# Optimization experiments

Measured on AMD Instinct MI355X. Metric: run time of the kernel, lower is better.

The kernel has to match this reference:

```python
import jax, jax.numpy as jnp
import numpy as np

EPS = 1e-5


def _layernorm(x, w, b):
    mu = jnp.mean(x, axis=-1, keepdims=True)
    xc = x - mu
    var = jnp.mean(xc * xc, axis=-1, keepdims=True)
    return xc * jax.lax.rsqrt(var + EPS) * w + b


def _s5_ssm(u, lam_re, lam_im, log_step, B_re, B_im, C_re, C_im, Dvec):
    # u: [B,L,D]; diagonal complex SSM with ZOH discretization + associative scan
    Lam = lam_re + 1j * lam_im                      # [P]
    step = jnp.exp(log_step)                        # [P]
    Abar = jnp.exp(Lam * step)                      # [P]
    Bbar = ((Abar - 1.0) / Lam)[:, None] * (B_re + 1j * B_im)  # [P,D]
    Bu = jnp.einsum('bld,pd->blp', u.astype(jnp.complex64), Bbar)  # [B,L,P]
    A_el = jnp.broadcast_to(Abar, Bu.shape)

    def binop(e1, e2):
        a1, b1 = e1
        a2, b2 = e2
        return a1 * a2, a2 * b1 + b2

    _, xs = jax.lax.associative_scan(binop, (A_el, Bu), axis=1)  # [B,L,P] complex
    y = jnp.einsum('blp,dp->bld', xs, C_re + 1j * C_im).real + Dvec * u
    return y


def _s5_block(x, an_w, an_b, lam_re, lam_im, log_step, B_re, B_im, C_re, C_im,
              Dvec, fn_w, fn_b, Wenc, Wdec):
    fx = _layernorm(x, an_w, an_b)
    s = _s5_ssm(fx, lam_re, lam_im, log_step, B_re, B_im, C_re, C_im, Dvec)
    z = jax.nn.gelu(s, approximate=False) + fx
    fy = _layernorm(z, fn_w, fn_b)
    h = fy @ Wenc.T                                  # [B,L,2D]
    a, g = jnp.split(h, 2, axis=-1)                  # GEGLU
    return (a * jax.nn.gelu(g, approximate=False)) @ Wdec.T + fy


def setup_inputs() -> dict:
    D = 1048   # d_model
    P = 1048   # state_dim
    NL = 3
    Bsz, L = 4, 4096
    key = jax.random.key(0)
    ks = jax.random.split(key, 20)
    f32 = jnp.float32
    inp = {}
    inp['x'] = jax.random.normal(ks[0], (Bsz, L, 1), f32)
    inp['enc_w'] = jax.random.normal(ks[1], (D, 1), f32)
    inp['enc_b'] = jnp.zeros((D,), f32)
    inp['norm_w'] = jnp.ones((NL, D), f32)
    inp['norm_b'] = jnp.zeros((NL, D), f32)
    inp['attn_norm_w'] = jnp.ones((NL, D), f32)
    inp['attn_norm_b'] = jnp.zeros((NL, D), f32)
    inp['ff_norm_w'] = jnp.ones((NL, D), f32)
    inp['ff_norm_b'] = jnp.zeros((NL, D), f32)
    # stable diagonal dynamics: Re(Lambda) < 0
    inp['lam_re'] = -0.5 * jax.random.uniform(ks[2], (NL, P), f32) - 0.05
    inp['lam_im'] = np.float32(np.pi) * jax.random.normal(ks[3], (NL, P), f32)
    lo, hi = np.float32(np.log(1e-3)), np.float32(np.log(1e-1))
    inp['log_step'] = lo + (hi - lo) * jax.random.uniform(ks[4], (NL, P), f32)
    sB = np.float32(1.0 / np.sqrt(D))
    sC = np.float32(1.0 / np.sqrt(P))
    inp['B_re'] = sB * jax.random.normal(ks[5], (NL, P, D), f32)
    inp['B_im'] = sB * jax.random.normal(ks[6], (NL, P, D), f32)
    inp['C_re'] = sC * jax.random.normal(ks[7], (NL, D, P), f32)
    inp['C_im'] = sC * jax.random.normal(ks[8], (NL, D, P), f32)
    inp['Dvec'] = jax.random.normal(ks[9], (NL, D), f32)
    sW = np.float32(1.0 / np.sqrt(D))
    inp['Wenc'] = sW * jax.random.normal(ks[10], (NL, 2 * D, D), f32)
    inp['Wdec'] = sW * jax.random.normal(ks[11], (NL, D, D), f32)
    inp['head_w'] = sW * jax.random.normal(ks[12], (1, D), f32)
    inp['head_b'] = jnp.zeros((1,), f32)
    return inp


def reference(x, enc_w, enc_b, norm_w, norm_b, attn_norm_w, attn_norm_b,
              ff_norm_w, ff_norm_b, lam_re, lam_im, log_step, B_re, B_im,
              C_re, C_im, Dvec, Wenc, Wdec, head_w, head_b):
    h = x @ enc_w.T + enc_b                          # [B,L,D]
    n_layers = norm_w.shape[0]
    for i in range(n_layers):                        # small fixed loop over layers
        z = _layernorm(h, norm_w[i], norm_b[i])      # prenorm
        z = _s5_block(z, attn_norm_w[i], attn_norm_b[i], lam_re[i], lam_im[i],
                      log_step[i], B_re[i], B_im[i], C_re[i], C_im[i],
                      Dvec[i], ff_norm_w[i], ff_norm_b[i], Wenc[i], Wdec[i])
        h = h + z                                    # residual (dropout = identity in eval)
    pooled = jnp.mean(h, axis=1)                     # [B,D]
    y = (pooled @ head_w.T + head_b).squeeze(-1)     # [B]
    return y
```

## Files before the change

### kernel.cpp

```cpp
#include <hip/hip_runtime.h>
#include <hip/hip_bf16.h>
#include <cstddef>

typedef __hip_bfloat16 bf16;

#define D_MODEL 1048
#define P_DIM   1048
#define NLAYER  3
#define BSZ     4
#define LSEQ    4096
#define BL      (BSZ*LSEQ)
#define BLD     ((size_t)BL*D_MODEL)
#define KP      1056
#define NP      1152
#define BLA     ((size_t)BL*KP)
#define NPKP    ((size_t)NP*KP)

#define NC      64
#define CL      (LSEQ/NC)
#define NSCAN   (BSZ*NC*P_DIM)
#define P2      (P_DIM/2)
#define NSCAN2  (BSZ*NC*P2)

typedef __attribute__((ext_vector_type(8))) short short8;
typedef __attribute__((ext_vector_type(4))) float f32x4;

#define TM 128
#define TN 128
#define TK 32
#define TILE_SH (TM*TK)
#define NGEMM   ((BL/TM)*(NP/TN))
#define KSTEPS  (KP/TK)

__device__ __forceinline__ float gelu_f(float x) {
    return 0.5f * x * (1.f + erff(x * 0.70710678118654752f));
}

__device__ __forceinline__ void tile_coords(int id, int& m0, int& n0) {
    int xcd  = id & 7;
    int slot = id >> 3;
    int xg   = slot / 9;
    int j    = slot - xg*9;
    m0 = (xg*8 + xcd) * TM;
    n0 = j * TN;
}

__device__ __forceinline__ void stage_tile(
    const bf16* __restrict__ src, int row0, int k0, short* lds, int tid)
{
#pragma unroll
    for (int c = 0; c < 2; ++c) {
        int chunk = tid + 256*c;
        int r = chunk >> 2;
        int col = ((chunk ^ (r >> 1)) & 3) * 8;
        __builtin_amdgcn_global_load_lds(
            (const __attribute__((address_space(1))) void*)(src + (size_t)(row0 + r)*KP + k0 + col),
            (__attribute__((address_space(3))) void*)(lds + chunk*8), 16, 0, 0);
    }
}

__device__ __forceinline__ void stage512(
    const bf16* __restrict__ src, int row0, int k0, short* lds, int tid)
{
    int r = tid >> 2;
    int col = ((tid ^ (r >> 1)) & 3) * 8;
    __builtin_amdgcn_global_load_lds(
        (const __attribute__((address_space(1))) void*)(src + (size_t)(row0 + r)*KP + k0 + col),
        (__attribute__((address_space(3))) void*)(lds + tid*8), 16, 0, 0);
}

__device__ __forceinline__ void mfma_step1(
    const short* As, const short* Ws, f32x4 (&acc)[4][4],
    int wm, int wn, int row_in, int qs)
{
    short8 a[4], b[4];
#pragma unroll
    for (int i = 0; i < 4; ++i) {
        a[i] = *(const short8*)&As[(wm + i*16 + row_in)*TK + qs];
        b[i] = *(const short8*)&Ws[(wn + i*16 + row_in)*TK + qs];
    }
#pragma unroll
    for (int i = 0; i < 4; ++i)
#pragma unroll
        for (int j = 0; j < 4; ++j)
            acc[i][j] = __builtin_amdgcn_mfma_f32_16x16x32_bf16(a[i], b[j], acc[i][j], 0, 0, 0);
}

template <int MODE>
__global__ __launch_bounds__(512, 4) void gemm2o_k(
    const bf16* __restrict__ A, const bf16* __restrict__ W0,
    const bf16* __restrict__ W1,
    bf16* __restrict__ O0, bf16* __restrict__ O1, int N)
{
    __shared__ __align__(16) short smem[6*TILE_SH];
    short* As  = smem;
    short* W0s = smem + 2*TILE_SH;
    short* W1s = smem + 4*TILE_SH;
    const int tid  = threadIdx.x;
    int m0, n0;
    tile_coords(blockIdx.x, m0, n0);
    const int wave = tid >> 6, lane = tid & 63;
    const int wr = wave >> 2, wc = wave & 3;
    const int wm = wr * 64;
    const int wn = (wc & 1) * 64;
    const bool useW1 = (wc >= 2);
    const int row_in = lane & 15;
    const int qs = (((lane >> 4) ^ (lane >> 1)) & 3) * 8;

    f32x4 acc[4][4] = {};

    stage512(A,  m0, 0,  As,             tid);
    stage512(W0, n0, 0,  W0s,            tid);
    stage512(W1, n0, 0,  W1s,            tid);
    stage512(A,  m0, 32, As  + TILE_SH,  tid);
    stage512(W0, n0, 32, W0s + TILE_SH,  tid);
    stage512(W1, n0, 32, W1s + TILE_SH,  tid);

    for (int s = 0; s < KSTEPS - 1; ++s) {
        asm volatile("s_waitcnt vmcnt(3)" ::: "memory");
        __builtin_amdgcn_s_barrier();
        const int off = (s & 1) * TILE_SH;
        const short* Ws = (useW1 ? W1s : W0s) + off;
        mfma_step1(As + off, Ws, acc, wm, wn, row_in, qs);
        __builtin_amdgcn_s_barrier();
        if (s < KSTEPS - 2) {
            const int k0 = (s + 2) * TK;
            stage512(A,  m0, k0, As  + off, tid);
            stage512(W0, n0, k0, W0s + off, tid);
            stage512(W1, n0, k0, W1s + off, tid);
        }
    }
    asm volatile("s_waitcnt vmcnt(0)" ::: "memory");
    __builtin_amdgcn_s_barrier();
    {
        const int off = ((KSTEPS-1) & 1) * TILE_SH;
        const short* Ws = (useW1 ? W1s : W0s) + off;
        mfma_step1(As + off, Ws, acc, wm, wn, row_in, qs);
    }

    const int quad = lane >> 4;
    if (MODE == 0) {
        bf16* O = useW1 ? O1 : O0;
#pragma unroll
        for (int i = 0; i < 4; ++i) {
#pragma unroll
            for (int j = 0; j < 4; ++j) {
                int n = n0 + wn + j*16 + row_in;
#pragma unroll
                for (int r = 0; r < 4; ++r) {
                    int m = m0 + wm + i*16 + quad*4 + r;
                    size_t o = (size_t)m*KP + n;
                    if (n < N)        O[o] = __float2bfloat16(acc[i][j][r]);
                    else if (n < KP)  O[o] = __float2bfloat16(0.f);
                }
            }
        }
    } else {
        f32x4* xb = (f32x4*)smem;
        const int pp = wr*2 + (wc & 1);
#pragma unroll
        for (int ih = 0; ih < 2; ++ih) {
            __syncthreads();
            if (useW1) {
#pragma unroll
                for (int il = 0; il < 2; ++il)
#pragma unroll
                    for (int j = 0; j < 4; ++j)
                        xb[(((pp*2 + il)*4 + j) << 6) + lane] = acc[2*ih + il][j];
            }
            __syncthreads();
            if (!useW1) {
#pragma unroll
                for (int il = 0; il < 2; ++il) {
                    int i = 2*ih + il;
#pragma unroll
                    for (int j = 0; j < 4; ++j) {
                        f32x4 g = xb[(((pp*2 + il)*4 + j) << 6) + lane];
                        int n = n0 + wn + j*16 + row_in;
#pragma unroll
                        for (int r = 0; r < 4; ++r) {
                            int m = m0 + wm + i*16 + quad*4 + r;
                            size_t o = (size_t)m*KP + n;
                            if (n < N)        O0[o] = __float2bfloat16(acc[i][j][r] * gelu_f(g[r]));
                            else if (n < KP)  O0[o] = __float2bfloat16(0.f);
                        }
                    }
                }
            }
        }
    }
}

__global__ __launch_bounds__(256, 3) void gemmC_k(
    const bf16* __restrict__ A0, const bf16* __restrict__ W0,
    const bf16* __restrict__ A1, const bf16* __restrict__ W1,
    const bf16* __restrict__ fx, const float* __restrict__ dv,
    bf16* __restrict__ O, int N)
{
    __shared__ __align__(16) short As[2][TILE_SH];
    __shared__ __align__(16) short Ws[2][TILE_SH];
    const int tid  = threadIdx.x;
    int m0, n0;
    tile_coords(blockIdx.x, m0, n0);
    const int wave = tid >> 6, lane = tid & 63;
    const int wm = (wave >> 1) * 64, wn = (wave & 1) * 64;
    const int row_in = lane & 15;
    const int qs = (((lane >> 4) ^ (lane >> 1)) & 3) * 8;

    f32x4 acc[4][4] = {};

    const int NST = 2*KSTEPS;
    stage_tile(A0, m0, 0,  As[0], tid);
    stage_tile(W0, n0, 0,  Ws[0], tid);
    stage_tile(A0, m0, 32, As[1], tid);
    stage_tile(W0, n0, 32, Ws[1], tid);

    for (int s = 0; s < NST - 1; ++s) {
        asm volatile("s_waitcnt vmcnt(4)" ::: "memory");
        __builtin_amdgcn_s_barrier();
        mfma_step1(As[s & 1], Ws[s & 1], acc, wm, wn, row_in, qs);
        __builtin_amdgcn_s_barrier();
        if (s < NST - 2) {
            int t = s + 2;
            const bf16* A = (t >= KSTEPS) ? A1 : A0;
            const bf16* W = (t >= KSTEPS) ? W1 : W0;
            int kk = (t >= KSTEPS) ? t - KSTEPS : t;
            stage_tile(A, m0, kk*TK, As[s & 1], tid);
            stage_tile(W, n0, kk*TK, Ws[s & 1], tid);
        }
    }
    asm volatile("s_waitcnt vmcnt(0)" ::: "memory");
    __builtin_amdgcn_s_barrier();
    mfma_step1(As[(NST-1) & 1], Ws[(NST-1) & 1], acc, wm, wn, row_in, qs);

    const int quad = lane >> 4;
#pragma unroll
    for (int i = 0; i < 4; ++i) {
#pragma unroll
        for (int j = 0; j < 4; ++j) {
            int n = n0 + wn + j*16 + row_in;
#pragma unroll
            for (int r = 0; r < 4; ++r) {
                int m = m0 + wm + i*16 + quad*4 + r;
                size_t o = (size_t)m*KP + n;
                if (n < N) {
                    float f = __bfloat162float(fx[o]);
                    float t = acc[i][j][r] + dv[n]*f;
                    O[o] = __float2bfloat16(gelu_f(t) + f);
                } else if (n < KP) {
                    O[o] = __float2bfloat16(0.f);
                }
            }
        }
    }
}

__global__ __launch_bounds__(256, 3) void gemmD_k(
    const bf16* __restrict__ A, const bf16* __restrict__ W,
    const bf16* __restrict__ fy, float* __restrict__ h, int N)
{
    __shared__ __align__(16) short As[2][TILE_SH];
    __shared__ __align__(16) short Ws[2][TILE_SH];
    const int tid  = threadIdx.x;
    int m0, n0;
    tile_coords(blockIdx.x, m0, n0);
    const int wave = tid >> 6, lane = tid & 63;
    const int wm = (wave >> 1) * 64, wn = (wave & 1) * 64;
    const int row_in = lane & 15;
    const int qs = (((lane >> 4) ^ (lane >> 1)) & 3) * 8;

    f32x4 acc[4][4] = {};

    stage_tile(A, m0, 0,  As[0], tid);
    stage_tile(W, n0, 0,  Ws[0], tid);
    stage_tile(A, m0, 32, As[1], tid);
    stage_tile(W, n0, 32, Ws[1], tid);

    for (int s = 0; s < KSTEPS - 1; ++s) {
        asm volatile("s_waitcnt vmcnt(4)" ::: "memory");
        __builtin_amdgcn_s_barrier();
        mfma_step1(As[s & 1], Ws[s & 1], acc, wm, wn, row_in, qs);
        __builtin_amdgcn_s_barrier();
        if (s < KSTEPS - 2) {
            const int k0 = (s + 2) * TK;
            stage_tile(A, m0, k0, As[s & 1], tid);
            stage_tile(W, n0, k0, Ws[s & 1], tid);
        }
    }
    asm volatile("s_waitcnt vmcnt(0)" ::: "memory");
    __builtin_amdgcn_s_barrier();
    mfma_step1(As[(KSTEPS-1) & 1], Ws[(KSTEPS-1) & 1], acc, wm, wn, row_in, qs);

    const int quad = lane >> 4;
#pragma unroll
    for (int i = 0; i < 4; ++i) {
#pragma unroll
        for (int j = 0; j < 4; ++j) {
            int n = n0 + wn + j*16 + row_in;
            if (n >= N) continue;
#pragma unroll
            for (int r = 0; r < 4; ++r) {
                int m = m0 + wm + i*16 + quad*4 + r;
                float f = __bfloat162float(fy[(size_t)m*KP + n]);
                h[(size_t)m*D_MODEL + n] += acc[i][j][r] + f;
            }
        }
    }
}

__global__ __launch_bounds__(256) void convw5_k(
    const float* __restrict__ s0, const float* __restrict__ s1,
    const float* __restrict__ s2, const float* __restrict__ s3,
    const float* __restrict__ s4, bf16* __restrict__ dst)
{
    size_t i = (size_t)blockIdx.x*256 + threadIdx.x;
    if (i >= NPKP) return;
    int z = blockIdx.z;
    const float* src = (z == 0) ? s0 : (z == 1) ? s1 : (z == 2) ? s2 : (z == 3) ? s3 : s4;
    float scale = (z == 1) ? -1.f : 1.f;
    int n = (int)(i / KP), k = (int)(i - (size_t)n*KP);
    float v = (n < D_MODEL && k < D_MODEL) ? scale*src[(size_t)n*D_MODEL + k] : 0.f;
    dst[(size_t)z*NPKP + i] = __float2bfloat16(v);
}

__device__ __forceinline__ float2 block_reduce2(float a, float b) {
    __syncthreads();
    for (int off = 32; off; off >>= 1) {
        a += __shfl_down(a, off, 64);
        b += __shfl_down(b, off, 64);
    }
    __shared__ float sa[4], sb[4];
    int lane = threadIdx.x & 63, wv = threadIdx.x >> 6;
    if (lane == 0) { sa[wv] = a; sb[wv] = b; }
    __syncthreads();
    if (threadIdx.x == 0) {
        sa[0] = sa[0]+sa[1]+sa[2]+sa[3];
        sb[0] = sb[0]+sb[1]+sb[2]+sb[3];
    }
    __syncthreads();
    return make_float2(sa[0], sb[0]);
}

template <int ENC>
__global__ __launch_bounds__(256) void ln2x_k(
    const float* __restrict__ xin,
    const float* __restrict__ ew, const float* __restrict__ eb,
    float* __restrict__ hbuf,
    const float* __restrict__ w1, const float* __restrict__ bb1,
    const float* __restrict__ w2, const float* __restrict__ bb2,
    bf16* __restrict__ y)
{
    const size_t row = blockIdx.x;
    float v[5];
    float s = 0.f, ss = 0.f;
    int i = 0;
    if (ENC) {
        float xv = xin[row];
        float* hr = hbuf + row * D_MODEL;
        for (int d = threadIdx.x; d < KP; d += 256, ++i) {
            float t = 0.f;
            if (d < D_MODEL) { t = xv*ew[d] + eb[d]; hr[d] = t; }
            v[i] = t; s += t; ss += t*t;
        }
    } else {
        const float* xr = hbuf + row * D_MODEL;
        for (int d = threadIdx.x; d < KP; d += 256, ++i) {
            float t = (d < D_MODEL) ? xr[d] : 0.f;
            v[i] = t; s += t; ss += t*t;
        }
    }
    float2 r = block_reduce2(s, ss);
    float mu  = r.x * (1.f/D_MODEL);
    float var = r.y * (1.f/D_MODEL) - mu*mu;
    float inv = rsqrtf(var + 1e-5f);
    s = 0.f; ss = 0.f; i = 0;
    for (int d = threadIdx.x; d < KP; d += 256, ++i) {
        float z = (d < D_MODEL) ? (v[i]-mu)*inv*w1[d] + bb1[d] : 0.f;
        v[i] = z; s += z; ss += z*z;
    }
    r = block_reduce2(s, ss);
    mu  = r.x * (1.f/D_MODEL);
    var = r.y * (1.f/D_MODEL) - mu*mu;
    inv = rsqrtf(var + 1e-5f);
    bf16* yr = y + row * KP;
    i = 0;
    for (int d = threadIdx.x; d < KP; d += 256, ++i) {
        float o = (d < D_MODEL) ? (v[i]-mu)*inv*w2[d] + bb2[d] : 0.f;
        yr[d] = __float2bfloat16(o);
    }
}

__global__ __launch_bounds__(256) void ln_k(
    const bf16* __restrict__ x, const float* __restrict__ w,
    const float* __restrict__ b, bf16* __restrict__ y)
{
    const size_t row = blockIdx.x;
    const bf16* xr = x + row * KP;
    float v[5];
    float s = 0.f, ss = 0.f;
    int i = 0;
    for (int d = threadIdx.x; d < KP; d += 256, ++i) {
        float t = (d < D_MODEL) ? __bfloat162float(xr[d]) : 0.f;
        v[i] = t; s += t; ss += t*t;
    }
    float2 r = block_reduce2(s, ss);
    float mu  = r.x * (1.f/D_MODEL);
    float var = r.y * (1.f/D_MODEL) - mu*mu;
    float inv = rsqrtf(var + 1e-5f);
    bf16* yr = y + row * KP;
    i = 0;
    for (int d = threadIdx.x; d < KP; d += 256, ++i) {
        float o = (d < D_MODEL) ? (v[i]-mu)*inv*w[d] + b[d] : 0.f;
        yr[d] = __float2bfloat16(o);
    }
}

__global__ __launch_bounds__(256) void prep_k(
    const float* __restrict__ lam_re, const float* __restrict__ lam_im,
    const float* __restrict__ log_step,
    const float* __restrict__ B_re, const float* __restrict__ B_im,
    bf16* __restrict__ bbar_re, bf16* __restrict__ bbar_im,
    float* __restrict__ abar)
{
    size_t idx = (size_t)blockIdx.x*256 + threadIdx.x;
    if (idx >= NPKP) return;
    int p = (int)(idx / KP);
    int d = (int)(idx - (size_t)p*KP);
    if (p >= P_DIM || d >= D_MODEL) {
        bbar_re[idx] = __float2bfloat16(0.f);
        bbar_im[idx] = __float2bfloat16(0.f);
        return;
    }
    float lr = lam_re[p], li = lam_im[p];
    float st = expf(log_step[p]);
    float er = expf(lr*st);
    float ar = er * cosf(li*st);
    float ai = er * sinf(li*st);
    if (d == 0) { abar[p] = ar; abar[P_DIM + p] = ai; }
    float den = lr*lr + li*li;
    float xr = ar - 1.f, xi = ai;
    float cr = (xr*lr + xi*li) / den;
    float ci = (xi*lr - xr*li) / den;
    float br = B_re[(size_t)p*D_MODEL + d], bi = B_im[(size_t)p*D_MODEL + d];
    bbar_re[idx] = __float2bfloat16(cr*br - ci*bi);
    bbar_im[idx] = __float2bfloat16(cr*bi + ci*br);
}

__device__ __forceinline__ float2 bf2f(unsigned int u) {
    unsigned int lo = u << 16, hi = u & 0xffff0000u;
    float2 r;
    r.x = __uint_as_float(lo);
    r.y = __uint_as_float(hi);
    return r;
}
__device__ __forceinline__ unsigned int f2bf2(float a, float b) {
    bf16 ba = __float2bfloat16(a), bb = __float2bfloat16(b);
    unsigned short ua = *(unsigned short*)&ba, ub = *(unsigned short*)&bb;
    return (unsigned int)ua | ((unsigned int)ub << 16);
}

__global__ __launch_bounds__(256) void scan_partial_k(
    const unsigned int* __restrict__ ur, const unsigned int* __restrict__ ui,
    const float* __restrict__ abar,
    float* __restrict__ sum_re, float* __restrict__ sum_im)
{
    int idx = blockIdx.x*256 + threadIdx.x;
    if (idx >= NSCAN2) return;
    int p2 = idx % P2;
    int rest = idx / P2;
    int c = rest % NC, b = rest / NC;
    int p = 2*p2;
    float ar0 = abar[p],   ai0 = abar[P_DIM + p];
    float ar1 = abar[p+1], ai1 = abar[P_DIM + p + 1];
    size_t base = (((size_t)b*LSEQ + (size_t)c*CL)*KP + p) >> 1;
    float s0r = 0.f, s0i = 0.f, s1r = 0.f, s1i = 0.f;
    for (int i = 0; i < CL; ++i) {
        size_t o = base + (size_t)i*(KP/2);
        float2 br = bf2f(ur[o]);
        float2 bi = bf2f(ui[o]);
        float n0r = fmaf(ar0, s0r, fmaf(-ai0, s0i, br.x));
        float n0i = fmaf(ar0, s0i, fmaf( ai0, s0r, bi.x));
        float n1r = fmaf(ar1, s1r, fmaf(-ai1, s1i, br.y));
        float n1i = fmaf(ar1, s1i, fmaf( ai1, s1r, bi.y));
        s0r = n0r; s0i = n0i; s1r = n1r; s1i = n1i;
    }
    size_t so = ((size_t)b*NC + c)*P_DIM + p;
    *(float2*)&sum_re[so] = make_float2(s0r, s1r);
    *(float2*)&sum_im[so] = make_float2(s0i, s1i);
}

__global__ __launch_bounds__(256) void scan_carry_k(
    const float* __restrict__ sum_re, const float* __restrict__ sum_im,
    const float* __restrict__ abar,
    float* __restrict__ car_re, float* __restrict__ car_im)
{
    int idx = blockIdx.x*256 + threadIdx.x;
    if (idx >= BSZ*P_DIM) return;
    int p = idx % P_DIM, b = idx / P_DIM;
    float cr = abar[p], ci = abar[P_DIM + p];
#pragma unroll
    for (int s = 0; s < 6; ++s) {
        float nr = cr*cr - ci*ci;
        float ni = 2.f*cr*ci;
        cr = nr; ci = ni;
    }
    float xre = 0.f, xim = 0.f;
    size_t base = (size_t)b*NC*P_DIM + p;
    for (int c = 0; c < NC; ++c) {
        size_t o = base + (size_t)c*P_DIM;
        car_re[o] = xre; car_im[o] = xim;
        float sre = sum_re[o], sim = sum_im[o];
        float nr = fmaf(cr, xre, fmaf(-ci, xim, sre));
        float ni = fmaf(cr, xim, fmaf( ci, xre, sim));
        xre = nr; xim = ni;
    }
}

__global__ __launch_bounds__(256) void scan_apply_k(
    unsigned int* __restrict__ ur, unsigned int* __restrict__ ui,
    const float* __restrict__ abar,
    const float* __restrict__ car_re, const float* __restrict__ car_im)
{
    int idx = blockIdx.x*256 + threadIdx.x;
    if (idx >= NSCAN2) return;
    int p2 = idx % P2;
    int rest = idx / P2;
    int c = rest % NC, b = rest / NC;
    int p = 2*p2;
    float ar0 = abar[p],   ai0 = abar[P_DIM + p];
    float ar1 = abar[p+1], ai1 = abar[P_DIM + p + 1];
    size_t co = ((size_t)b*NC + c)*P_DIM + p;
    float2 c_r = *(const float2*)&car_re[co];
    float2 c_i = *(const float2*)&car_im[co];
    float x0r = c_r.x, x0i = c_i.x, x1r = c_r.y, x1i = c_i.y;
    size_t base = (((size_t)b*LSEQ + (size_t)c*CL)*KP + p) >> 1;
    for (int i = 0; i < CL; ++i) {
        size_t o = base + (size_t)i*(KP/2);
        float2 br = bf2f(ur[o]);
        float2 bi = bf2f(ui[o]);
        float n0r = fmaf(ar0, x0r, fmaf(-ai0, x0i, br.x));
        float n0i = fmaf(ar0, x0i, fmaf( ai0, x0r, bi.x));
        float n1r = fmaf(ar1, x1r, fmaf(-ai1, x1i, br.y));
        float n1i = fmaf(ar1, x1i, fmaf( ai1, x1r, bi.y));
        x0r = n0r; x0i = n0i; x1r = n1r; x1i = n1i;
        ur[o] = f2bf2(x0r, x1r);
        ui[o] = f2bf2(x0i, x1i);
    }
}

__global__ void head_init_k(float* out, const float* hb)
{
    if (threadIdx.x < BSZ) out[threadIdx.x] = hb[0];
}

__global__ __launch_bounds__(256) void head_k(
    const float* __restrict__ h, const float* __restrict__ hw,
    float* __restrict__ out)
{
    int b = blockIdx.x;
    int chunk = blockIdx.y;
    const float* hb = h + ((size_t)b*LSEQ + (size_t)chunk*64)*D_MODEL;
    float s = 0.f;
    for (int l = 0; l < 64; ++l) {
        const float* hr = hb + (size_t)l*D_MODEL;
        for (int d = threadIdx.x; d < D_MODEL; d += 256)
            s += hr[d]*hw[d];
    }
    for (int off = 32; off; off >>= 1) s += __shfl_down(s, off, 64);
    __shared__ float sm[4];
    int lane = threadIdx.x & 63, wv = threadIdx.x >> 6;
    if (lane == 0) sm[wv] = s;
    __syncthreads();
    if (threadIdx.x == 0)
        atomicAdd(out + b, (sm[0]+sm[1]+sm[2]+sm[3]) * (1.f/LSEQ));
}

extern "C" void kernel_launch(void* const* d_in, const int* in_sizes, int n_in,
                              void* d_out, int out_size, void* d_ws, size_t ws_size,
                              hipStream_t stream)
{
    const float* x          = (const float*)d_in[0];
    const float* enc_w      = (const float*)d_in[1];
    const float* enc_b      = (const float*)d_in[2];
    const float* norm_w     = (const float*)d_in[3];
    const float* norm_b     = (const float*)d_in[4];
    const float* attn_w     = (const float*)d_in[5];
    const float* attn_b     = (const float*)d_in[6];
    const float* ff_w       = (const float*)d_in[7];
    const float* ff_b       = (const float*)d_in[8];
    const float* lam_re     = (const float*)d_in[9];
    const float* lam_im     = (const float*)d_in[10];
    const float* log_step   = (const float*)d_in[11];
    const float* B_re       = (const float*)d_in[12];
    const float* B_im       = (const float*)d_in[13];
    const float* C_re       = (const float*)d_in[14];
    const float* C_im       = (const float*)d_in[15];
    const float* Dvec       = (const float*)d_in[16];
    const float* Wenc       = (const float*)d_in[17];
    const float* Wdec       = (const float*)d_in[18];
    const float* head_w     = (const float*)d_in[19];
    const float* head_b     = (const float*)d_in[20];
    float* out = (float*)d_out;

    float* h    = (float*)d_ws;
    bf16*  b1   = (bf16*)(h + BLD);
    bf16*  b2   = b1 + BLA;
    bf16*  b3   = b2 + BLA;
    bf16*  b4   = b3 + BLA;
    bf16*  wbr  = b4 + BLA;
    bf16*  wbi  = wbr + NPKP;
    bf16*  w5   = wbi + NPKP;
    bf16*  wcr  = w5;
    bf16*  wci  = w5 + NPKP;
    bf16*  wea  = w5 + 2*NPKP;
    bf16*  weg  = w5 + 3*NPKP;
    bf16*  wd   = w5 + 4*NPKP;
    float* abar = (float*)(w5 + 5*NPKP);
    float* sum_re = abar + 2*P_DIM;
    float* sum_im = sum_re + NSCAN;
    float* car_re = sum_im + NSCAN;
    float* car_im = car_re + NSCAN;

    const int CV   = (int)((NPKP + 255)/256);
    const int SC_G = (NSCAN2 + 255)/256;
    const size_t pd = (size_t)P_DIM*D_MODEL;

    for (int i = 0; i < NLAYER; ++i) {
        prep_k<<<CV, 256, 0, stream>>>(
            lam_re + i*P_DIM, lam_im + i*P_DIM, log_step + i*P_DIM,
            B_re + i*pd, B_im + i*pd, wbr, wbi, abar);
        const float* WencA = Wenc + (size_t)i*2*pd;
        const float* WencG = WencA + pd;
        convw5_k<<<dim3(CV,1,5), 256, 0, stream>>>(
            C_re + i*pd, C_im + i*pd, WencA, WencG, Wdec + i*pd, w5);

        if (i == 0)
            ln2x_k<1><<<BL, 256, 0, stream>>>(x, enc_w, enc_b, h,
                norm_w + i*D_MODEL, norm_b + i*D_MODEL,
                attn_w + i*D_MODEL, attn_b + i*D_MODEL, b2);
        else
            ln2x_k<0><<<BL, 256, 0, stream>>>(nullptr, nullptr, nullptr, h,
                norm_w + i*D_MODEL, norm_b + i*D_MODEL,
                attn_w + i*D_MODEL, attn_b + i*D_MODEL, b2);

        gemm2o_k<0><<<NGEMM, 512, 0, stream>>>(b2, wbr, wbi, b1, b3, P_DIM);

        scan_partial_k<<<SC_G, 256, 0, stream>>>((unsigned int*)b1, (unsigned int*)b3,
                                                 abar, sum_re, sum_im);
        scan_carry_k<<<(BSZ*P_DIM + 255)/256, 256, 0, stream>>>(sum_re, sum_im, abar, car_re, car_im);
        scan_apply_k<<<SC_G, 256, 0, stream>>>((unsigned int*)b1, (unsigned int*)b3,
                                               abar, car_re, car_im);

        gemmC_k<<<NGEMM, 256, 0, stream>>>(b1, wcr, b3, wci, b2, Dvec + i*D_MODEL, b4, D_MODEL);

        ln_k<<<BL, 256, 0, stream>>>(b4, ff_w + i*D_MODEL, ff_b + i*D_MODEL, b1);

        gemm2o_k<1><<<NGEMM, 512, 0, stream>>>(b1, wea, weg, b2, nullptr, D_MODEL);

        gemmD_k<<<NGEMM, 256, 0, stream>>>(b2, wd, b1, h, D_MODEL);
    }

    head_init_k<<<1, 64, 0, stream>>>(out, head_b);
    head_k<<<dim3(BSZ, 64), 256, 0, stream>>>(h, head_w, out);
}
```

Baseline: 2.080 ms.

## Triple-buffer dual-output GEMM, lower GEMM occupancy hints, fuse weight prep kernels

The gemm2o kernel moves from double to triple buffering of its A, W0 and W1 shared-memory tiles, rotating buffer pointers and waiting on fewer outstanding loads, so global loads are issued further ahead of the MFMA work. The launch-bounds occupancy hint for gemmC and gemmD drops from 3 to 2 blocks per SM, giving the compiler more registers at the cost of fewer resident blocks. The prep_k and convw5_k kernels are merged into one launch with an extra grid z-slice, saving one launch per layer. The larger shared-memory footprint in gemm2o may lower its occupancy.

```diff
diff --git a/kernel.cpp b/kernel.cpp
--- a/kernel.cpp
+++ b/kernel.cpp
@@ -86,16 +86,18 @@
             acc[i][j] = __builtin_amdgcn_mfma_f32_16x16x32_bf16(a[i], b[j], acc[i][j], 0, 0, 0);
 }
 
+#define ROT3(p0, p1, p2) { short* _t = p0; p0 = p1; p1 = p2; p2 = _t; }
+
 template <int MODE>
 __global__ __launch_bounds__(512, 4) void gemm2o_k(
     const bf16* __restrict__ A, const bf16* __restrict__ W0,
     const bf16* __restrict__ W1,
     bf16* __restrict__ O0, bf16* __restrict__ O1, int N)
 {
-    __shared__ __align__(16) short smem[6*TILE_SH];
-    short* As  = smem;
-    short* W0s = smem + 2*TILE_SH;
-    short* W1s = smem + 4*TILE_SH;
+    __shared__ __align__(16) short smem[9*TILE_SH];
+    short *pA  = smem,             *pA1  = smem + TILE_SH,   *pA2  = smem + 2*TILE_SH;
+    short *pW0 = smem + 3*TILE_SH, *pW01 = smem + 4*TILE_SH, *pW02 = smem + 5*TILE_SH;
+    short *pW1 = smem + 6*TILE_SH, *pW11 = smem + 7*TILE_SH, *pW12 = smem + 8*TILE_SH;
     const int tid  = threadIdx.x;
     int m0, n0;
     tile_coords(blockIdx.x, m0, n0);
@@ -109,34 +111,38 @@
 
     f32x4 acc[4][4] = {};
 
-    stage512(A,  m0, 0,  As,             tid);
-    stage512(W0, n0, 0,  W0s,            tid);
-    stage512(W1, n0, 0,  W1s,            tid);
-    stage512(A,  m0, 32, As  + TILE_SH,  tid);
-    stage512(W0, n0, 32, W0s + TILE_SH,  tid);
-    stage512(W1, n0, 32, W1s + TILE_SH,  tid);
-
-    for (int s = 0; s < KSTEPS - 1; ++s) {
-        asm volatile("s_waitcnt vmcnt(3)" ::: "memory");
+    stage512(A,  m0, 0,    pA,   tid);
+    stage512(W0, n0, 0,    pW0,  tid);
+    stage512(W1, n0, 0,    pW1,  tid);
+    stage512(A,  m0, TK,   pA1,  tid);
+    stage512(W0, n0, TK,   pW01, tid);
+    stage512(W1, n0, TK,   pW11, tid);
+    stage512(A,  m0, 2*TK, pA2,  tid);
+    stage512(W0, n0, 2*TK, pW02, tid);
+    stage512(W1, n0, 2*TK, pW12, tid);
+
+    for (int s = 0; s <= KSTEPS - 4; ++s) {
+        asm volatile("s_waitcnt vmcnt(6)" ::: "memory");
         __builtin_amdgcn_s_barrier();
-        const int off = (s & 1) * TILE_SH;
-        const short* Ws = (useW1 ? W1s : W0s) + off;
-        mfma_step1(As + off, Ws, acc, wm, wn, row_in, qs);
+        mfma_step1(pA, useW1 ? pW1 : pW0, acc, wm, wn, row_in, qs);
         __builtin_amdgcn_s_barrier();
-        if (s < KSTEPS - 2) {
-            const int k0 = (s + 2) * TK;
-            stage512(A,  m0, k0, As  + off, tid);
-            stage512(W0, n0, k0, W0s + off, tid);
-            stage512(W1, n0, k0, W1s + off, tid);
-        }
-    }
+        const int k0 = (s + 3) * TK;
+        stage512(A,  m0, k0, pA,  tid);
+        stage512(W0, n0, k0, pW0, tid);
+        stage512(W1, n0, k0, pW1, tid);
+        ROT3(pA,  pA1,  pA2);
+        ROT3(pW0, pW01, pW02);
+        ROT3(pW1, pW11, pW12);
+    }
+    asm volatile("s_waitcnt vmcnt(6)" ::: "memory");
+    __builtin_amdgcn_s_barrier();
+    mfma_step1(pA, useW1 ? pW1 : pW0, acc, wm, wn, row_in, qs);
+    asm volatile("s_waitcnt vmcnt(3)" ::: "memory");
+    __builtin_amdgcn_s_barrier();
+    mfma_step1(pA1, useW1 ? pW11 : pW01, acc, wm, wn, row_in, qs);
     asm volatile("s_waitcnt vmcnt(0)" ::: "memory");
     __builtin_amdgcn_s_barrier();
-    {
-        const int off = ((KSTEPS-1) & 1) * TILE_SH;
-        const short* Ws = (useW1 ? W1s : W0s) + off;
-        mfma_step1(As + off, Ws, acc, wm, wn, row_in, qs);
-    }
+    mfma_step1(pA2, useW1 ? pW12 : pW02, acc, wm, wn, row_in, qs);
 
     const int quad = lane >> 4;
     if (MODE == 0) {
@@ -191,7 +197,7 @@
     }
 }
 
-__global__ __launch_bounds__(256, 3) void gemmC_k(
+__global__ __launch_bounds__(256, 2) void gemmC_k(
     const bf16* __restrict__ A0, const bf16* __restrict__ W0,
     const bf16* __restrict__ A1, const bf16* __restrict__ W1,
     const bf16* __restrict__ fx, const float* __restrict__ dv,
@@ -212,8 +218,8 @@
     const int NST = 2*KSTEPS;
     stage_tile(A0, m0, 0,  As[0], tid);
     stage_tile(W0, n0, 0,  Ws[0], tid);
-    stage_tile(A0, m0, 32, As[1], tid);
-    stage_tile(W0, n0, 32, Ws[1], tid);
+    stage_tile(A0, m0, TK, As[1], tid);
+    stage_tile(W0, n0, TK, Ws[1], tid);
 
     for (int s = 0; s < NST - 1; ++s) {
         asm volatile("s_waitcnt vmcnt(4)" ::: "memory");
@@ -255,7 +261,7 @@
     }
 }
 
-__global__ __launch_bounds__(256, 3) void gemmD_k(
+__global__ __launch_bounds__(256, 2) void gemmD_k(
     const bf16* __restrict__ A, const bf16* __restrict__ W,
     const bf16* __restrict__ fy, float* __restrict__ h, int N)
 {
@@ -273,8 +279,8 @@
 
     stage_tile(A, m0, 0,  As[0], tid);
     stage_tile(W, n0, 0,  Ws[0], tid);
-    stage_tile(A, m0, 32, As[1], tid);
-    stage_tile(W, n0, 32, Ws[1], tid);
+    stage_tile(A, m0, TK, As[1], tid);
+    stage_tile(W, n0, TK, Ws[1], tid);
 
     for (int s = 0; s < KSTEPS - 1; ++s) {
         asm volatile("s_waitcnt vmcnt(4)" ::: "memory");
@@ -308,19 +314,47 @@
     }
 }
 
-__global__ __launch_bounds__(256) void convw5_k(
+__global__ __launch_bounds__(256) void prepconv_k(
+    const float* __restrict__ lam_re, const float* __restrict__ lam_im,
+    const float* __restrict__ log_step,
+    const float* __restrict__ B_re, const float* __restrict__ B_im,
+    bf16* __restrict__ bbar_re, bf16* __restrict__ bbar_im,
+    float* __restrict__ abar,
     const float* __restrict__ s0, const float* __restrict__ s1,
     const float* __restrict__ s2, const float* __restrict__ s3,
-    const float* __restrict__ s4, bf16* __restrict__ dst)
-{
-    size_t i = (size_t)blockIdx.x*256 + threadIdx.x;
-    if (i >= NPKP) return;
+    const float* __restrict__ s4, bf16* __restrict__ w5)
+{
+    size_t idx = (size_t)blockIdx.x*256 + threadIdx.x;
+    if (idx >= NPKP) return;
     int z = blockIdx.z;
-    const float* src = (z == 0) ? s0 : (z == 1) ? s1 : (z == 2) ? s2 : (z == 3) ? s3 : s4;
-    float scale = (z == 1) ? -1.f : 1.f;
-    int n = (int)(i / KP), k = (int)(i - (size_t)n*KP);
-    float v = (n < D_MODEL && k < D_MODEL) ? scale*src[(size_t)n*D_MODEL + k] : 0.f;
-    dst[(size_t)z*NPKP + i] = __float2bfloat16(v);
+    int p = (int)(idx / KP);
+    int d = (int)(idx - (size_t)p*KP);
+    if (z == 0) {
+        if (p >= P_DIM || d >= D_MODEL) {
+            bbar_re[idx] = __float2bfloat16(0.f);
+            bbar_im[idx] = __float2bfloat16(0.f);
+            return;
+        }
+        float lr = lam_re[p], li = lam_im[p];
+        float st = expf(log_step[p]);
+        float er = expf(lr*st);
+        float ar = er * cosf(li*st);
+        float ai = er * sinf(li*st);
+        if (d == 0) { abar[p] = ar; abar[P_DIM + p] = ai; }
+        float den = lr*lr + li*li;
+        float xr = ar - 1.f, xi = ai;
+        float cr = (xr*lr + xi*li) / den;
+        float ci = (xi*lr - xr*li) / den;
+        float br = B_re[(size_t)p*D_MODEL + d], bi = B_im[(size_t)p*D_MODEL + d];
+        bbar_re[idx] = __float2bfloat16(cr*br - ci*bi);
+        bbar_im[idx] = __float2bfloat16(cr*bi + ci*br);
+    } else {
+        int w = z - 1;
+        const float* src = (w == 0) ? s0 : (w == 1) ? s1 : (w == 2) ? s2 : (w == 3) ? s3 : s4;
+        float scale = (w == 1) ? -1.f : 1.f;
+        float v = (p < D_MODEL && d < D_MODEL) ? scale*src[(size_t)p*D_MODEL + d] : 0.f;
+        w5[(size_t)w*NPKP + idx] = __float2bfloat16(v);
+    }
 }
 
 __device__ __forceinline__ float2 block_reduce2(float a, float b) {
@@ -413,37 +447,6 @@
         float o = (d < D_MODEL) ? (v[i]-mu)*inv*w[d] + b[d] : 0.f;
         yr[d] = __float2bfloat16(o);
     }
-}
-
-__global__ __launch_bounds__(256) void prep_k(
-    const float* __restrict__ lam_re, const float* __restrict__ lam_im,
-    const float* __restrict__ log_step,
-    const float* __restrict__ B_re, const float* __restrict__ B_im,
-    bf16* __restrict__ bbar_re, bf16* __restrict__ bbar_im,
-    float* __restrict__ abar)
-{
-    size_t idx = (size_t)blockIdx.x*256 + threadIdx.x;
-    if (idx >= NPKP) return;
-    int p = (int)(idx / KP);
-    int d = (int)(idx - (size_t)p*KP);
-    if (p >= P_DIM || d >= D_MODEL) {
-        bbar_re[idx] = __float2bfloat16(0.f);
-        bbar_im[idx] = __float2bfloat16(0.f);
-        return;
-    }
-    float lr = lam_re[p], li = lam_im[p];
-    float st = expf(log_step[p]);
-    float er = expf(lr*st);
-    float ar = er * cosf(li*st);
-    float ai = er * sinf(li*st);
-    if (d == 0) { abar[p] = ar; abar[P_DIM + p] = ai; }
-    float den = lr*lr + li*li;
-    float xr = ar - 1.f, xi = ai;
-    float cr = (xr*lr + xi*li) / den;
-    float ci = (xi*lr - xr*li) / den;
-    float br = B_re[(size_t)p*D_MODEL + d], bi = B_im[(size_t)p*D_MODEL + d];
-    bbar_re[idx] = __float2bfloat16(cr*br - ci*bi);
-    bbar_im[idx] = __float2bfloat16(cr*bi + ci*br);
 }
 
 __device__ __forceinline__ float2 bf2f(unsigned int u) {
@@ -626,12 +629,11 @@
     const size_t pd = (size_t)P_DIM*D_MODEL;
 
     for (int i = 0; i < NLAYER; ++i) {
-        prep_k<<<CV, 256, 0, stream>>>(
-            lam_re + i*P_DIM, lam_im + i*P_DIM, log_step + i*P_DIM,
-            B_re + i*pd, B_im + i*pd, wbr, wbi, abar);
         const float* WencA = Wenc + (size_t)i*2*pd;
         const float* WencG = WencA + pd;
-        convw5_k<<<dim3(CV,1,5), 256, 0, stream>>>(
+        prepconv_k<<<dim3(CV,1,6), 256, 0, stream>>>(
+            lam_re + i*P_DIM, lam_im + i*P_DIM, log_step + i*P_DIM,
+            B_re + i*pd, B_im + i*pd, wbr, wbi, abar,
             C_re + i*pd, C_im + i*pd, WencA, WencG, Wdec + i*pd, w5);
 
         if (i == 0)
```

New measurement: 1.916 ms, median of 2. 1.09x faster.
